# Performance work log

Measured on AMD Instinct MI355X. Metric: run time of the kernel, lower is better.

The kernel has to match this reference:

```python
import jax, jax.numpy as jnp
import numpy as np

B, H, W = 32, 128, 128
NA = 9            # number of anchors
STRIDE = 16.0
CLS_THRESH = 0.95
MAX_IOU = 0.1
NUM_PROP = 10
NEG = -1e9        # sentinel for suppressed / below-threshold scores


def setup_inputs() -> dict:
    key = jax.random.key(0)
    inputs = jax.random.normal(key, (B, H, W, NA * 4 + NA + 1), dtype=jnp.float32)
    anchors = jnp.array([[0.5, 32.0], [1.0, 32.0], [2.0, 32.0],
                         [0.5, 64.0], [1.0, 64.0], [2.0, 64.0],
                         [0.5, 128.0], [1.0, 128.0], [2.0, 128.0]], dtype=jnp.float32)
    return {"inputs": inputs, "anchors": anchors}


def _decode(inputs, anchors):
    b, h, w, c = inputs.shape
    cls = inputs[..., -1]
    # zero out 1-pixel border (the tf.pad'ed cancel matrix)
    border = jnp.zeros((h, w), inputs.dtype).at[1:-1, 1:-1].set(1.0)
    cls = cls * border
    a_reg = inputs[..., -10:-1]           # [B,H,W,9]
    bbox_reg = inputs[..., :-10]          # [B,H,W,36]
    a_idx = jnp.argmax(a_reg, axis=-1)    # [B,H,W] best anchor per position
    # gather the 4 deltas of the chosen anchor: channels a_idx*4 .. a_idx*4+3
    gidx = a_idx[..., None] * 4 + jnp.arange(4)
    deltas = jnp.take_along_axis(bbox_reg, gidx, axis=-1)          # [B,H,W,4]
    anc = anchors[a_idx].astype(jnp.float32)                       # [B,H,W,2]
    # anchor box: center x from column, center y from row, height=anc[:,1], width=anc[:,1]/anc[:,0]
    ax = (jnp.arange(w, dtype=jnp.float32)[None, :] + 0.5) * STRIDE  # [1,W]
    ay = (jnp.arange(h, dtype=jnp.float32)[:, None] + 0.5) * STRIDE  # [H,1]
    a0 = jnp.broadcast_to(ax, (h, w))[None]                          # [1,H,W]
    a1 = jnp.broadcast_to(ay, (h, w))[None]
    a2 = anc[..., 1]
    a3 = anc[..., 1] / anc[..., 0]
    b0 = deltas[..., 0] * a2 + a0
    b1 = deltas[..., 1] * a3 + a1
    b2 = jnp.exp(deltas[..., 2]) * a2
    b3 = jnp.exp(deltas[..., 3]) * a3
    bboxes = jnp.stack([b0, b1, b2, b3], axis=-1)                    # [B,H,W,4]
    coords = jnp.stack([b1 - b3 / 2, b0 - b2 / 2,
                        b1 + b3 / 2, b0 + b2 / 2], axis=-1)          # [y1,x1,y2,x2]
    scores = jnp.where(cls > CLS_THRESH, cls, NEG)                   # mask below-threshold
    n = h * w
    return (bboxes.reshape(b, n, 4), coords.reshape(b, n, 4), scores.reshape(b, n))


def _nms_one(boxes, coords, scores):
    # greedy NMS, equivalent to tf.image.non_max_suppression over the valid candidates
    n = scores.shape[0]
    area = jnp.maximum(coords[:, 2] - coords[:, 0], 0.0) * jnp.maximum(coords[:, 3] - coords[:, 1], 0.0)
    idx_range = jnp.arange(n)

    def body(i, state):
        sc, out = state
        j = jnp.argmax(sc)
        ok = sc[j] > NEG / 2
        sel = coords[j]
        iy1 = jnp.maximum(coords[:, 0], sel[0])
        ix1 = jnp.maximum(coords[:, 1], sel[1])
        iy2 = jnp.minimum(coords[:, 2], sel[2])
        ix2 = jnp.minimum(coords[:, 3], sel[3])
        inter = jnp.maximum(iy2 - iy1, 0.0) * jnp.maximum(ix2 - ix1, 0.0)
        area_s = jnp.maximum(sel[2] - sel[0], 0.0) * jnp.maximum(sel[3] - sel[1], 0.0)
        iou = inter / (area + area_s - inter + 1e-10)
        suppress = (iou > MAX_IOU) | (idx_range == j)
        sc = jnp.where(ok & suppress, NEG, sc)
        out = out.at[i].set(jnp.where(ok, boxes[j], jnp.zeros(4, boxes.dtype)))
        return sc, out

    out0 = jnp.zeros((NUM_PROP, 4), boxes.dtype)
    _, out = jax.lax.fori_loop(0, NUM_PROP, body, (scores, out0))
    return out


def _forward(inputs, anchors):
    bboxes, coords, scores = _decode(inputs, anchors)
    return jax.vmap(_nms_one)(bboxes, coords, scores)   # [B, NUM_PROP, 4]


def reference(inputs, anchors):
    return _forward(inputs, anchors)
```

## Files before the change

### kernel.cpp

```cpp
#include <hip/hip_runtime.h>
#include <math.h>

#define BB 32
#define HH 128
#define WW 128
#define NA 9
#define CCH 46
#define NPIX (HH*WW)
#define STRIDE_F 16.0f
#define CLS_T 0.95f
#define MAX_IOU_F 0.1f
#define NUM_PROP 10
#define NEGV -1000000000.0f

#define TILE_PIX 256
#define TILE_FLOATS (TILE_PIX * CCH)
#define TILE_VEC (TILE_FLOATS / 4)

#define NTILE (BB * NPIX / TILE_PIX)
#define NWAVES (NTILE * 4)
#define WSLOT 64

#define NMS_T 512
#define MAXPER 10
#define MMAX (MAXPER * NMS_T)

#define GLL16(gp, lp)                                                          \
  __builtin_amdgcn_global_load_lds(                                            \
      (__attribute__((address_space(1))) void*)(gp),                           \
      (__attribute__((address_space(3))) void*)(lp), 16, 0, 0)

__global__ __launch_bounds__(256, 3) void decode_kernel(
    const float* __restrict__ in, const float* __restrict__ anchors,
    int* __restrict__ wcnt, float* __restrict__ sc_comp,
    float4* __restrict__ co_comp)
{
  __shared__ float s_in[TILE_FLOATS];

  int tid = threadIdx.x;
  int tile = blockIdx.x;
  int g0 = tile * TILE_PIX;

  const float4* srcv = (const float4*)(in + (size_t)g0 * CCH);
  float4* dstv = (float4*)s_in;
#pragma unroll
  for (int i = 0; i < 12; ++i) {
    int k = tid + i * 256;
    if (k < TILE_VEC)
      GLL16(srcv + k, dstv + k);
  }
  __syncthreads();

  int g = g0 + tid;
  int p = g & (NPIX - 1);
  int h = p >> 7;
  int w = p & (WW - 1);
  const float* px = s_in + tid * CCH;

  float cls = px[45];
  bool interior = (h >= 1) && (h <= HH - 2) && (w >= 1) && (w <= WW - 2);
  bool cand = interior && (cls > CLS_T);

  unsigned long long mask = __ballot(cand);
  int lane = tid & 63;
  int waveid = tile * 4 + (tid >> 6);
  int total = __popcll(mask);
  if (lane == 0) wcnt[waveid] = total;

  if (!cand) return;

  int ai = 0; float av = px[36];
#pragma unroll
  for (int c = 1; c < NA; ++c) { float v = px[36 + c]; if (v > av) { av = v; ai = c; } }

  float d0 = px[ai * 4 + 0], d1 = px[ai * 4 + 1];
  float d2 = px[ai * 4 + 2], d3 = px[ai * 4 + 3];
  float ratio = anchors[ai * 2 + 0], sz = anchors[ai * 2 + 1];
  float a2 = sz, a3 = sz / ratio;
  float ax = ((float)w + 0.5f) * STRIDE_F;
  float ay = ((float)h + 0.5f) * STRIDE_F;
  float b0 = d0 * a2 + ax;
  float b1 = d1 * a3 + ay;
  float b2 = expf(d2) * a2;
  float b3 = expf(d3) * a3;
  float4 co = make_float4(b1 - 0.5f * b3, b0 - 0.5f * b2,
                          b1 + 0.5f * b3, b0 + 0.5f * b2);

  int prefix = __popcll(mask & ((1ull << lane) - 1ull));
  int slot = waveid * WSLOT + prefix;
  sc_comp[slot] = cls;
  co_comp[slot] = co;
}

__global__ __launch_bounds__(NMS_T, 1) void nms_kernel(
    const int* __restrict__ wcnt, const float* __restrict__ sc_comp,
    const float4* __restrict__ co_comp, float* __restrict__ out)
{
  __shared__ float  s_sc[MMAX];
  __shared__ float4 s_co[MMAX];
  __shared__ int    s_tmp[256];
  __shared__ float  s_rv[8];
  __shared__ int    s_rk[8];
  __shared__ float  s_jv;
  __shared__ int    s_jk;

  int b = blockIdx.x, tid = threadIdx.x;

  int c = 0;
  if (tid < 256) { c = wcnt[b * 256 + tid]; s_tmp[tid] = c; }
  __syncthreads();
  for (int d = 1; d < 256; d <<= 1) {
    int v = 0;
    if (tid < 256) { v = s_tmp[tid]; if (tid >= d) v += s_tmp[tid - d]; }
    __syncthreads();
    if (tid < 256) s_tmp[tid] = v;
    __syncthreads();
  }
  if (tid < 256) {
    int excl = s_tmp[tid] - c;
    const float*  sp = sc_comp + (size_t)(b * 256 + tid) * WSLOT;
    const float4* cp = co_comp + (size_t)(b * 256 + tid) * WSLOT;
    for (int i = 0; i < c; ++i) {
      int d = excl + i;
      if (d < MMAX) { s_sc[d] = sp[i]; s_co[d] = cp[i]; }
    }
  }
  __syncthreads();
  int M = s_tmp[255]; if (M > MMAX) M = MMAX;

  float  sc[MAXPER];
  float4 co[MAXPER];
  float  ar[MAXPER];
#pragma unroll
  for (int r = 0; r < MAXPER; ++r) {
    int k = r * NMS_T + tid;
    if (k < M) {
      sc[r] = s_sc[k];
      co[r] = s_co[k];
      ar[r] = fmaxf(co[r].z - co[r].x, 0.f) * fmaxf(co[r].w - co[r].y, 0.f);
    } else {
      sc[r] = NEGV; co[r] = make_float4(0.f, 0.f, 0.f, 0.f); ar[r] = 0.f;
    }
  }

  for (int it = 0; it < NUM_PROP; ++it) {
    float bv = -INFINITY; int bk = 0x7fffffff;
#pragma unroll
    for (int r = 0; r < MAXPER; ++r) {
      if (sc[r] > bv) { bv = sc[r]; bk = r * NMS_T + tid; }
    }
    for (int off = 32; off > 0; off >>= 1) {
      float ov = __shfl_down(bv, off);
      int   ok_ = __shfl_down(bk, off);
      if (ov > bv || (ov == bv && ok_ < bk)) { bv = ov; bk = ok_; }
    }
    int wv = tid >> 6;
    if ((tid & 63) == 0) { s_rv[wv] = bv; s_rk[wv] = bk; }
    __syncthreads();
    if (tid == 0) {
      float fv = s_rv[0]; int fk = s_rk[0];
#pragma unroll
      for (int q = 1; q < 8; ++q) {
        if (s_rv[q] > fv || (s_rv[q] == fv && s_rk[q] < fk)) { fv = s_rv[q]; fk = s_rk[q]; }
      }
      s_jv = fv; s_jk = fk;
    }
    __syncthreads();
    float jv = s_jv;
    bool okq = jv > (NEGV * 0.5f);

    if (okq) {
      int jk = s_jk;
      float4 selc = s_co[jk];
      float sy1 = selc.x, sx1 = selc.y, sy2 = selc.z, sx2 = selc.w;
      float sarea = fmaxf(sy2 - sy1, 0.f) * fmaxf(sx2 - sx1, 0.f);
#pragma unroll
      for (int r = 0; r < MAXPER; ++r) {
        float4 cc = co[r];
        float iy1 = fmaxf(cc.x, sy1);
        float ix1 = fmaxf(cc.y, sx1);
        float iy2 = fminf(cc.z, sy2);
        float ix2 = fminf(cc.w, sx2);
        float inter = fmaxf(iy2 - iy1, 0.f) * fmaxf(ix2 - ix1, 0.f);
        float iou = inter / (ar[r] + sarea - inter + 1e-10f);
        if (iou > MAX_IOU_F || (r * NMS_T + tid) == jk) sc[r] = NEGV;
      }
      if (tid == 0) {
        float* o = out + (size_t)(b * NUM_PROP + it) * 4;
        o[0] = 0.5f * (sx1 + sx2);
        o[1] = 0.5f * (sy1 + sy2);
        o[2] = sx2 - sx1;
        o[3] = sy2 - sy1;
      }
    } else if (tid == 0) {
      float* o = out + (size_t)(b * NUM_PROP + it) * 4;
      o[0] = 0.f; o[1] = 0.f; o[2] = 0.f; o[3] = 0.f;
    }
    __syncthreads();
  }
}

extern "C" void kernel_launch(void* const* d_in, const int* in_sizes, int n_in,
                              void* d_out, int out_size, void* d_ws, size_t ws_size,
                              hipStream_t stream) {
  const float* in      = (const float*)d_in[0];
  const float* anchors = (const float*)d_in[1];
  float* out = (float*)d_out;

  char* ws = (char*)d_ws;
  int*    wcnt    = (int*)ws;
  float4* co_comp = (float4*)(ws + (size_t)NWAVES * 4);
  float*  sc_comp = (float*)(ws + (size_t)NWAVES * 4 + (size_t)NWAVES * WSLOT * 16);

  decode_kernel<<<NTILE, 256, 0, stream>>>(in, anchors, wcnt, sc_comp, co_comp);
  nms_kernel<<<BB, NMS_T, 0, stream>>>(wcnt, sc_comp, co_comp, out);
}
```

Before: 171.5 us.

## Per-wave tile loads without block barrier; wave-shuffle scan and parallel gather in NMS

In the decode kernel each wave now loads only its own 64 pixels into LDS and waits on its own vmcnt, so the block-wide barrier is dropped and waves can start decoding independently. In the NMS kernel the 256-entry prefix sum over per-wave counts becomes a single-wave shuffle scan instead of a multi-barrier LDS scan. The serial per-thread compaction loop is replaced by all threads gathering candidates in parallel, each locating its source wave by binary search. This adds per-element search work and relies on the inline waitcnt being enough to make the async LDS writes visible.

```diff
diff --git a/kernel.cpp b/kernel.cpp
--- a/kernel.cpp
+++ b/kernel.cpp
@@ -15,7 +15,7 @@
 
 #define TILE_PIX 256
 #define TILE_FLOATS (TILE_PIX * CCH)
-#define TILE_VEC (TILE_FLOATS / 4)
+#define WAVE_VEC 736
 
 #define NTILE (BB * NPIX / TILE_PIX)
 #define NWAVES (NTILE * 4)
@@ -38,32 +38,33 @@
   __shared__ float s_in[TILE_FLOATS];
 
   int tid = threadIdx.x;
+  int lane = tid & 63;
+  int wv = tid >> 6;
   int tile = blockIdx.x;
   int g0 = tile * TILE_PIX;
-
-  const float4* srcv = (const float4*)(in + (size_t)g0 * CCH);
-  float4* dstv = (float4*)s_in;
-#pragma unroll
-  for (int i = 0; i < 12; ++i) {
-    int k = tid + i * 256;
-    if (k < TILE_VEC)
-      GLL16(srcv + k, dstv + k);
-  }
-  __syncthreads();
-
-  int g = g0 + tid;
+  int gw = g0 + wv * 64;
+
+  const float4* srcv = (const float4*)(in + (size_t)gw * CCH);
+  float4* dstv = (float4*)(s_in + (size_t)wv * 64 * CCH);
+#pragma unroll
+  for (int i = 0; i < 11; ++i)
+    GLL16(srcv + i * 64 + lane, dstv + i * 64 + lane);
+  if (lane < 32)
+    GLL16(srcv + 11 * 64 + lane, dstv + 11 * 64 + lane);
+  __asm__ volatile("s_waitcnt vmcnt(0)" ::: "memory");
+
+  int g = gw + lane;
   int p = g & (NPIX - 1);
   int h = p >> 7;
   int w = p & (WW - 1);
-  const float* px = s_in + tid * CCH;
+  const float* px = s_in + (size_t)(wv * 64 + lane) * CCH;
 
   float cls = px[45];
   bool interior = (h >= 1) && (h <= HH - 2) && (w >= 1) && (w <= WW - 2);
   bool cand = interior && (cls > CLS_T);
 
   unsigned long long mask = __ballot(cand);
-  int lane = tid & 63;
-  int waveid = tile * 4 + (tid >> 6);
+  int waveid = tile * 4 + wv;
   int total = __popcll(mask);
   if (lane == 0) wcnt[waveid] = total;
 
@@ -98,35 +99,43 @@
 {
   __shared__ float  s_sc[MMAX];
   __shared__ float4 s_co[MMAX];
-  __shared__ int    s_tmp[256];
+  __shared__ int    s_ps[256];
   __shared__ float  s_rv[8];
   __shared__ int    s_rk[8];
   __shared__ float  s_jv;
   __shared__ int    s_jk;
 
   int b = blockIdx.x, tid = threadIdx.x;
-
-  int c = 0;
-  if (tid < 256) { c = wcnt[b * 256 + tid]; s_tmp[tid] = c; }
+  int lane = tid & 63;
+
+  if (tid < 64) {
+    const int* wc = wcnt + b * 256 + tid * 4;
+    int c0 = wc[0], c1 = wc[1], c2 = wc[2], c3 = wc[3];
+    int l0 = c0, l1 = l0 + c1, l2 = l1 + c2, l3 = l2 + c3;
+    int sum = l3;
+    for (int off = 1; off < 64; off <<= 1) {
+      int v = __shfl_up(sum, off);
+      if (lane >= off) sum += v;
+    }
+    int excl = sum - l3;
+    s_ps[tid * 4 + 0] = excl + l0;
+    s_ps[tid * 4 + 1] = excl + l1;
+    s_ps[tid * 4 + 2] = excl + l2;
+    s_ps[tid * 4 + 3] = excl + l3;
+  }
   __syncthreads();
-  for (int d = 1; d < 256; d <<= 1) {
-    int v = 0;
-    if (tid < 256) { v = s_tmp[tid]; if (tid >= d) v += s_tmp[tid - d]; }
-    __syncthreads();
-    if (tid < 256) s_tmp[tid] = v;
-    __syncthreads();
-  }
-  if (tid < 256) {
-    int excl = s_tmp[tid] - c;
-    const float*  sp = sc_comp + (size_t)(b * 256 + tid) * WSLOT;
-    const float4* cp = co_comp + (size_t)(b * 256 + tid) * WSLOT;
-    for (int i = 0; i < c; ++i) {
-      int d = excl + i;
-      if (d < MMAX) { s_sc[d] = sp[i]; s_co[d] = cp[i]; }
-    }
+  int M = s_ps[255]; if (M > MMAX) M = MMAX;
+
+  for (int d = tid; d < M; d += NMS_T) {
+    int lo = 0, hi = 255;
+#pragma unroll
+    for (int s = 0; s < 8; ++s) { int mid = (lo + hi) >> 1; if (s_ps[mid] > d) hi = mid; else lo = mid + 1; }
+    int excl = (lo == 0) ? 0 : s_ps[lo - 1];
+    size_t src = (size_t)(b * 256 + lo) * WSLOT + (d - excl);
+    s_sc[d] = sc_comp[src];
+    s_co[d] = co_comp[src];
   }
   __syncthreads();
-  int M = s_tmp[255]; if (M > MMAX) M = MMAX;
 
   float  sc[MAXPER];
   float4 co[MAXPER];
@@ -155,7 +164,7 @@
       if (ov > bv || (ov == bv && ok_ < bk)) { bv = ov; bk = ok_; }
     }
     int wv = tid >> 6;
-    if ((tid & 63) == 0) { s_rv[wv] = bv; s_rk[wv] = bk; }
+    if (lane == 0) { s_rv[wv] = bv; s_rk[wv] = bk; }
     __syncthreads();
     if (tid == 0) {
       float fv = s_rv[0]; int fk = s_rk[0];
```

Result: no change. 172.3 us (+0.5%).
